# Kernel tuning notes

Hardware: AMD Instinct MI355X
Metric: run time of the kernel (lower is better)

## Reference

```python
import jax, jax.numpy as jnp
import numpy as np

N_EMBD = 1024
N_HEAD = 16
HEAD_DIM = N_EMBD // N_HEAD

def setup_inputs() -> dict:
    key = jax.random.key(0)
    ks = jax.random.split(key, 9)
    B, T, C = 2, 2048, N_EMBD
    s = 1.0 / np.sqrt(C)
    x = jax.random.normal(ks[0], (B, T, C), dtype=jnp.float32)
    Wk = jax.random.normal(ks[1], (C, C), dtype=jnp.float32) * s
    bk = jnp.zeros((C,), dtype=jnp.float32)
    Wq = jax.random.normal(ks[2], (C, C), dtype=jnp.float32) * s
    bq = jnp.zeros((C,), dtype=jnp.float32)
    Wv = jax.random.normal(ks[3], (C, C), dtype=jnp.float32) * s
    bv = jnp.zeros((C,), dtype=jnp.float32)
    Wp = jax.random.normal(ks[4], (C, C), dtype=jnp.float32) * s
    bp = jnp.zeros((C,), dtype=jnp.float32)
    return {"x": x, "Wq": Wq, "bq": bq, "Wk": Wk, "bk": bk, "Wv": Wv, "bv": bv, "Wp": Wp, "bp": bp}

def reference(x, Wq, bq, Wk, bk, Wv, bv, Wp, bp):
    B, T, C = x.shape
    H, D = N_HEAD, HEAD_DIM
    # QKV projections (torch Linear: x @ W.T + b; here W is stored as (in,out))
    q = (x @ Wq + bq).reshape(B, T, H, D).transpose(0, 2, 1, 3)  # [B,H,T,D]
    k = (x @ Wk + bk).reshape(B, T, H, D).transpose(0, 2, 1, 3)
    v = (x @ Wv + bv).reshape(B, T, H, D).transpose(0, 2, 1, 3)
    att = jnp.einsum('bhtd,bhsd->bhts', q, k) / jnp.sqrt(jnp.float32(D))
    causal = jnp.tril(jnp.ones((T, T), dtype=bool))
    att = jnp.where(causal, att, jnp.float32(-jnp.inf))
    att = jax.nn.softmax(att, axis=-1)
    y = jnp.einsum('bhts,bhsd->bhtd', att, v)  # [B,H,T,D]
    y = y.transpose(0, 2, 1, 3).reshape(B, T, C)
    return y @ Wp + bp
```

## Files before the change

### kernel.cpp

```cpp
#include <hip/hip_runtime.h>
#include <cstdint>

typedef __attribute__((ext_vector_type(4))) short s16x4;
typedef __attribute__((ext_vector_type(8))) short s16x8;
typedef __attribute__((ext_vector_type(4))) float f32x4;
typedef __attribute__((ext_vector_type(16))) float f32x16;

#define L2E 1.44269504088896340736f

__device__ __forceinline__ short f2bf(float f) {
  union { float f; unsigned u; } v; v.f = f;
  unsigned r = (v.u + 0x7fffu + ((v.u >> 16) & 1u)) >> 16;
  return (short)r;
}

__device__ __forceinline__ float xhalf_f(float x) {
  union { float f; unsigned u; } a; a.f = x;
  auto r = __builtin_amdgcn_permlane32_swap(a.u, a.u, false, false);
  union { unsigned u; float f; } b;
  b.u = (threadIdx.x & 32) ? r[0] : r[1];
  return b.f;
}

typedef const __attribute__((address_space(1))) unsigned int* gas_p;
typedef __attribute__((address_space(3))) unsigned int* las_p;
__device__ __forceinline__ void stage16(const void* g, void* l) {
  __builtin_amdgcn_global_load_lds((gas_p)(uintptr_t)g,
                                   (las_p)(unsigned int)(uintptr_t)l, 16, 0, 0);
}

__global__ __launch_bounds__(256) void prepass(const float* __restrict__ W0,
                                               const float* __restrict__ W1,
                                               const float* __restrict__ W2,
                                               const float* __restrict__ W3,
                                               short* __restrict__ wdst,
                                               const float* __restrict__ x,
                                               short* __restrict__ xb) {
  const int z = blockIdx.z;
  const int t = threadIdx.x;
  if (z >= 4) {
    int i = ((z - 4) * 256 + blockIdx.y * 16 + blockIdx.x) * 256 + t;
    const f32x4* p = (const f32x4*)x + (size_t)i * 2;
    f32x4 a = p[0], b = p[1];
    s16x8 o;
    o[0] = f2bf(a[0]); o[1] = f2bf(a[1]); o[2] = f2bf(a[2]); o[3] = f2bf(a[3]);
    o[4] = f2bf(b[0]); o[5] = f2bf(b[1]); o[6] = f2bf(b[2]); o[7] = f2bf(b[3]);
    *((s16x8*)xb + i) = o;
    return;
  }
  __shared__ float tile[64][65];
  const float* in = (z == 0) ? W0 : (z == 1) ? W1 : (z == 2) ? W2 : W3;
  short* out = wdst + (size_t)z * 1048576;
  const int bi = blockIdx.y, bj = blockIdx.x;
  const int c = t & 63, r0 = t >> 6;
#pragma unroll
  for (int i = 0; i < 16; i++) {
    int r = r0 + i * 4;
    tile[r][c] = in[(size_t)(bi * 64 + r) * 1024 + bj * 64 + c];
  }
  __syncthreads();
#pragma unroll
  for (int i = 0; i < 16; i++) {
    int r = r0 + i * 4;
    out[(size_t)(bj * 64 + r) * 1024 + bi * 64 + c] = f2bf(tile[c][r]);
  }
}

__global__ __launch_bounds__(512) void gemm_qkv8(
    const short* __restrict__ A, const short* __restrict__ B,
    const float* __restrict__ b0, const float* __restrict__ b1,
    const float* __restrict__ b2, short* __restrict__ o0,
    short* __restrict__ o1, short* __restrict__ o2) {
  constexpr int K = 1024, NKT = 16;
  constexpr int BUFS = 28672;
  __shared__ short L[2 * BUFS];
  const int tid = threadIdx.x;
  const int lane = tid & 63, wave = tid >> 6;
  const int wr = wave >> 2, wc = wave & 3;
  const int l15 = lane & 15, l4 = lane >> 4;
  const int id = blockIdx.x;
  const int wgid = (id & 7) * 32 + (id >> 3);
  const int m0 = (wgid & 15) * 256;
  const int n0 = (wgid >> 4) * 192;
  const short* Asrc = A + (size_t)m0 * K;
  const short* Bsrc = B + (size_t)n0 * K;

  f32x4 acc[8][3];
#pragma unroll
  for (int i = 0; i < 8; i++)
#pragma unroll
    for (int j = 0; j < 3; j++) acc[i][j] = (f32x4){0.f, 0.f, 0.f, 0.f};

  int sALo[2], gALo[2], sBLo[2], gBLo[2];
#pragma unroll
  for (int j = 0; j < 2; j++) {
    const int flat = j * 512 + tid;
    const int r = flat >> 3, ch = flat & 7;
    const int sw8 = ((ch ^ (r & 7)) << 3);
    sALo[j] = (r >> 6) * 8192 + (r & 63) * 64 + (ch << 3);
    gALo[j] = ((r >> 6) * 128 + (r & 63)) * K + sw8;
    sBLo[j] = 16384 + (flat << 3);
    gBLo[j] = r * K + sw8;
  }
  const int rBH = 128 + (tid >> 3), chBH = tid & 7;
  const int sBHi = 16384 + rBH * 64 + (chBH << 3);
  const int gBHi = rBH * K + ((chBH ^ (rBH & 7)) << 3);

  int aoff[2], boff[2];
#pragma unroll
  for (int kf = 0; kf < 2; kf++) {
    const int x = (((kf << 2) + l4) ^ (l15 & 7)) << 3;
    aoff[kf] = wr * 8192 + l15 * 64 + x;
    boff[kf] = 16384 + (wc * 48 + l15) * 64 + x;
  }

#define ST_ALO(BB, T)                                                          \
  { _Pragma("unroll") for (int j_ = 0; j_ < 2; j_++)                           \
        stage16(Asrc + gALo[j_] + (T)*64, L + (BB) + sALo[j_]); }
#define ST_AHI(BB, T)                                                          \
  { _Pragma("unroll") for (int j_ = 0; j_ < 2; j_++)                           \
        stage16(Asrc + gALo[j_] + 64 * K + (T)*64, L + (BB) + sALo[j_] + 4096); }
#define ST_BLO(BB, T)                                                          \
  { _Pragma("unroll") for (int j_ = 0; j_ < 2; j_++)                           \
        stage16(Bsrc + gBLo[j_] + (T)*64, L + (BB) + sBLo[j_]); }
#define ST_BHI(BB, T)                                                          \
  stage16(Bsrc + gBHi + (T)*64, L + (BB) + sBHi);

#define RD_A(MI0)                                                              \
  { _Pragma("unroll") for (int q_ = 0; q_ < 2; q_++)                           \
        _Pragma("unroll") for (int kf_ = 0; kf_ < 2; kf_++)                    \
            af[q_][kf_] = *(const s16x8*)(bc + aoff[kf_] + ((MI0) + q_) * 1024); }

#define BAR_MFMA(MI0)                                                          \
  __builtin_amdgcn_s_barrier();                                                \
  asm volatile("s_waitcnt lgkmcnt(0)" ::: "memory");                           \
  __builtin_amdgcn_sched_barrier(0);                                           \
  __builtin_amdgcn_s_setprio(1);                                               \
  _Pragma("unroll") for (int q_ = 0; q_ < 2; q_++)                             \
      _Pragma("unroll") for (int ni_ = 0; ni_ < 3; ni_++)                      \
          _Pragma("unroll") for (int kf_ = 0; kf_ < 2; kf_++)                  \
              acc[(MI0) + q_][ni_] = __builtin_amdgcn_mfma_f32_16x16x32_bf16(  \
                  af[q_][kf_], bf[ni_][kf_], acc[(MI0) + q_][ni_], 0, 0, 0);   \
  __builtin_amdgcn_s_setprio(0);                                               \
  __builtin_amdgcn_s_barrier();

  ST_ALO(0, 0) ST_AHI(0, 0) ST_BLO(0, 0) ST_BHI(0, 0)
  ST_BLO(BUFS, 1) ST_BHI(BUFS, 1) ST_ALO(BUFS, 1)
  asm volatile("s_waitcnt vmcnt(5)" ::: "memory");
  __builtin_amdgcn_s_barrier();

  int bufc = 0;
  for (int t = 0; t < NKT; ++t) {
    const int bufn = bufc ^ BUFS;
    const short* bc = L + bufc;
    s16x8 bf[3][2], af[2][2];
#pragma unroll
    for (int ni_ = 0; ni_ < 3; ni_++)
#pragma unroll
      for (int kf_ = 0; kf_ < 2; kf_++)
        bf[ni_][kf_] = *(const s16x8*)(bc + boff[kf_] + ni_ * 1024);
    RD_A(0)
    if (t + 1 < NKT) ST_AHI(bufn, t + 1)
    BAR_MFMA(0)
    RD_A(2)
    if (t + 2 < NKT) ST_BLO(bufc, t + 2)
    BAR_MFMA(2)
    RD_A(4)
    if (t + 2 < NKT) ST_BHI(bufc, t + 2)
    BAR_MFMA(4)
    RD_A(6)
    if (t + 2 < NKT) {
      ST_ALO(bufc, t + 2)
      asm volatile("s_waitcnt vmcnt(5)" ::: "memory");
    } else {
      asm volatile("s_waitcnt vmcnt(0)" ::: "memory");
    }
    BAR_MFMA(6)
    bufc = bufn;
  }
#undef ST_ALO
#undef ST_AHI
#undef ST_BLO
#undef ST_BHI
#undef RD_A
#undef BAR_MFMA

#pragma unroll
  for (int ni = 0; ni < 3; ni++) {
    const int col = n0 + wc * 48 + ni * 16 + l15;
    const float* bp; short* dst; int c1; int isV = 0; float scl = 1.0f;
    if (col < 1024) { bp = b0; dst = o0; c1 = col; scl = 0.125f * L2E; }
    else if (col < 2048) { bp = b1; dst = o1; c1 = col - 1024; }
    else { bp = b2; dst = o2; c1 = col - 2048; isV = 1; }
    const float bias = bp[c1];
    const int h = c1 >> 6, d = c1 & 63;
    if (isV) {
#pragma unroll
      for (int mi = 0; mi < 8; mi++) {
        int t0 = m0 + wr * 128 + mi * 16 + l4 * 4;
        int bb = t0 >> 11, tt = t0 & 2047;
        s16x4 ov;
#pragma unroll
        for (int rr = 0; rr < 4; rr++) ov[rr] = f2bf(acc[mi][ni][rr] + bias);
        *(s16x4*)(dst + (size_t)((bb * 16 + h) * 64 + d) * 2048 + tt) = ov;
      }
    } else {
#pragma unroll
      for (int mi = 0; mi < 8; mi++)
#pragma unroll
        for (int rr = 0; rr < 4; rr++) {
          int row = m0 + wr * 128 + mi * 16 + l4 * 4 + rr;
          int bb = row >> 11, tt = row & 2047;
          float v = (acc[mi][ni][rr] + bias) * scl;
          dst[(size_t)((bb * 16 + h) * 2048 + tt) * 64 + d] = f2bf(v);
        }
    }
  }
}

template <int EPI, int BM>
__global__ __launch_bounds__(BM * 2) void gemm_bt(
    const short* __restrict__ A, const short* __restrict__ B, int N, int K,
    const float* __restrict__ b0, float* __restrict__ ofp) {
  constexpr int T = BM * 2;
  constexpr int AR = 2;
  constexpr int BR = 512 / T;
  constexpr int BUFB = (BM + 128) * 32;
  __shared__ short L[2 * BUFB];
  const int tid = threadIdx.x;
  const int lane = tid & 63;
  const int wave = tid >> 6;
  const int wr = wave >> 1, wc = wave & 1;
  const int l15 = lane & 15, l4 = lane >> 4;
  const int id = blockIdx.x + gridDim.x * blockIdx.y;
  const int cpx = gridDim.x >> 3;
  const int xcd = id & 7, sub = id >> 3;
  const int m0 = (sub / cpx) * BM;
  const int n0 = (xcd * cpx + sub % cpx) * 128;
  f32x4 acc[4][4];
#pragma unroll
  for (int i = 0; i < 4; i++)
#pragma unroll
    for (int j = 0; j < 4; j++) acc[i][j] = (f32x4){0.f, 0.f, 0.f, 0.f};

  const int lq = tid & 3, lr = tid >> 2;
  int soffA[AR], goffA[AR];
#pragma unroll
  for (int i = 0; i < AR; i++) {
    const int r = i * (T / 4) + lr;
    soffA[i] = r * 32 + lq * 8;
    goffA[i] = r * K + lq * 8;
  }
  int soffB[BR], goffB[BR];
#pragma unroll
  for (int j = 0; j < BR; j++) {
    const int r = j * (T / 4) + lr;
    soffB[j] = BM * 32 + r * 32 + lq * 8;
    goffB[j] = r * K + lq * 8;
  }

  const short* Asrc = A + (size_t)m0 * K;
  const short* Bsrc = B + (size_t)n0 * K;
  short* bufC = L;
  short* bufN = L + BUFB;

#define GSTAGE(BUF)                                                            \
  {                                                                            \
    _Pragma("unroll") for (int i_ = 0; i_ < AR; i_++)                          \
        stage16(Asrc + goffA[i_], (BUF) + soffA[i_]);                          \
    _Pragma("unroll") for (int j_ = 0; j_ < BR; j_++)                          \
        stage16(Bsrc + goffB[j_], (BUF) + soffB[j_]);                          \
    Asrc += 32; Bsrc += 32;                                                    \
  }

  GSTAGE(bufC)
  const int NK = K >> 5;
  for (int kt = 0; kt < NK; kt++) {
    __syncthreads();
    if (kt + 1 < NK) GSTAGE(bufN)
    s16x8 af[4], bfr[4];
#pragma unroll
    for (int i = 0; i < 4; i++) {
      af[i] = *(const s16x8*)(bufC + (wr * 64 + i * 16 + l15) * 32 + l4 * 8);
      bfr[i] = *(const s16x8*)(bufC + BM * 32 + (wc * 64 + i * 16 + l15) * 32 + l4 * 8);
    }
#pragma unroll
    for (int mi = 0; mi < 4; mi++)
#pragma unroll
      for (int ni = 0; ni < 4; ni++)
        acc[mi][ni] = __builtin_amdgcn_mfma_f32_16x16x32_bf16(af[mi], bfr[ni],
                                                              acc[mi][ni], 0, 0, 0);
    short* t_ = bufC; bufC = bufN; bufN = t_;
  }
#undef GSTAGE

#pragma unroll
  for (int ni = 0; ni < 4; ni++) {
    const int col = n0 + wc * 64 + ni * 16 + l15;
    const float bias = b0[col];
#pragma unroll
    for (int mi = 0; mi < 4; mi++)
#pragma unroll
      for (int r = 0; r < 4; r++) {
        int row = m0 + wr * 64 + mi * 16 + l4 * 4 + r;
        ofp[(size_t)row * N + col] = acc[mi][ni][r] + bias;
      }
  }
}

__global__ __launch_bounds__(128) void attn_v8(const short* __restrict__ Q,
                                               const short* __restrict__ K,
                                               const short* __restrict__ Vt,
                                               short* __restrict__ Y) {
  __shared__ short Ks[2][64 * 64];
  __shared__ short Vs[3][64 * 64];
  const int bh = blockIdx.x;
  const int y = blockIdx.y;
  const int g = y >> 3, r_ = y & 7;
  const int qbase = (g << 3) | ((g & 1) ? (7 - r_) : r_);
  const int qt = (qbase + ((bh & 3) << 3)) & 31;
  const int tid = threadIdx.x, lane = tid & 63, wave = tid >> 6;
  const int q31 = lane & 31, hi = lane >> 5;
  const short* Qp = Q + (size_t)bh * 2048 * 64;
  const short* Kp = K + (size_t)bh * 2048 * 64;
  const short* Vp = Vt + (size_t)bh * 64 * 2048;
  const int qrow = qt * 64 + wave * 32 + q31;
  const int nt = qt + 1;
  const int cx = q31 & 7;

  s16x8 qf[4];
#pragma unroll
  for (int s = 0; s < 4; s++)
    qf[s] = *(const s16x8*)(Qp + (size_t)qrow * 64 + s * 16 + hi * 8);

  f32x16 accA, accB, Z;
#pragma unroll
  for (int i = 0; i < 16; i++) { accA[i] = 0.f; accB[i] = 0.f; Z[i] = 0.f; }
  float l = 0.f;

  const int srow = tid >> 3, sch = tid & 7;
  int sdst[4], koff[4], voff[4];
#pragma unroll
  for (int i = 0; i < 4; i++) {
    const int r = srow + i * 16;
    const int sc = sch ^ (r & 7);
    sdst[i] = r * 64 + sch * 8;
    koff[i] = r * 64 + sc * 8;
    voff[i] = r * 2048 + sc * 8;
  }
  const short* kst = Kp;
  const short* vst = Vp;
  int rd0[4];
#pragma unroll
  for (int s = 0; s < 4; s++) rd0[s] = q31 * 64 + (((2 * s + hi) ^ cx) << 3);

  short* kA = &Ks[0][0]; short* kB = &Ks[1][0];
  short* vP = &Vs[2][0]; short* vC = &Vs[0][0]; short* vN = &Vs[1][0];

#pragma unroll
  for (int i = 0; i < 4; i++) {
    stage16(kst + koff[i], kA + sdst[i]);
    stage16(vst + voff[i], vC + sdst[i]);
  }
  kst += 4096; vst += 64;

#define STAGE_NEXT(COND)                                                       \
  if (COND) {                                                                  \
    _Pragma("unroll") for (int i_ = 0; i_ < 4; i_++) {                         \
      stage16(kst + koff[i_], kB + sdst[i_]);                                  \
      stage16(vst + voff[i_], vN + sdst[i_]);                                  \
    }                                                                          \
    kst += 4096; vst += 64;                                                    \
  }

#define QK(S0, S1)                                                             \
  {                                                                            \
    s16x8 kf0_[4], kf1_[4];                                                    \
    _Pragma("unroll") for (int s_ = 0; s_ < 4; s_++) {                         \
      kf0_[s_] = *(const s16x8*)(kA + rd0[s_]);                                \
      kf1_[s_] = *(const s16x8*)(kA + rd0[s_] + 2048);                         \
    }                                                                          \
    __builtin_amdgcn_s_setprio(1);                                             \
    S0 = __builtin_amdgcn_mfma_f32_32x32x16_bf16(kf0_[0], qf[0], Z, 0, 0, 0);  \
    S1 = __builtin_amdgcn_mfma_f32_32x32x16_bf16(kf1_[0], qf[0], Z, 0, 0, 0);  \
    _Pragma("unroll") for (int s_ = 1; s_ < 4; s_++) {                         \
      S0 = __builtin_amdgcn_mfma_f32_32x32x16_bf16(kf0_[s_], qf[s_], S0, 0, 0, 0); \
      S1 = __builtin_amdgcn_mfma_f32_32x32x16_bf16(kf1_[s_], qf[s_], S1, 0, 0, 0); \
    }                                                                          \
    __builtin_amdgcn_s_setprio(0);                                             \
  }

#define SMPV_BODY(S0, S1)                                                      \
  {                                                                            \
    float rsum_ = 0.f;                                                         \
    _Pragma("unroll") for (int r2_ = 0; r2_ < 16; r2_++) {                     \
      float p_ = __builtin_amdgcn_exp2f(S0[r2_]);                              \
      S0[r2_] = p_; rsum_ += p_;                                               \
    }                                                                          \
    _Pragma("unroll") for (int r2_ = 0; r2_ < 16; r2_++) {                     \
      float p_ = __builtin_amdgcn_exp2f(S1[r2_]);                              \
      S1[r2_] = p_; rsum_ += p_;                                               \
    }                                                                          \
    l += rsum_;                                                                \
    unsigned pk0_[8], pk1_[8];                                                 \
    _Pragma("unroll") for (int j_ = 0; j_ < 8; j_++) {                         \
      unsigned u_;                                                             \
      float a0_ = S0[2 * j_], a1_ = S0[2 * j_ + 1];                            \
      asm("v_cvt_pk_bf16_f32 %0, %1, %2" : "=v"(u_) : "v"(a0_), "v"(a1_));     \
      pk0_[j_] = u_;                                                           \
      float b0_ = S1[2 * j_], b1_ = S1[2 * j_ + 1];                            \
      asm("v_cvt_pk_bf16_f32 %0, %1, %2" : "=v"(u_) : "v"(b0_), "v"(b1_));     \
      pk1_[j_] = u_;                                                           \
    }                                                                          \
    _Pragma("unroll") for (int s_ = 0; s_ < 4; s_++) {                         \
      const unsigned* pk_ = (s_ < 2) ? pk0_ : pk1_;                            \
      const int b_ = 4 * (s_ & 1);                                             \
      auto rA_ = __builtin_amdgcn_permlane32_swap(pk_[b_ + 0], pk_[b_ + 2], false, false); \
      auto rB_ = __builtin_amdgcn_permlane32_swap(pk_[b_ + 1], pk_[b_ + 3], false, false); \
      union { unsigned u[4]; s16x8 v; } fr_;                                   \
      fr_.u[0] = rA_[0]; fr_.u[1] = rB_[0]; fr_.u[2] = rA_[1]; fr_.u[3] = rB_[1]; \
      s16x8 vf0_ = *(const s16x8*)(vP + rd0[s_]);                              \
      s16x8 vf1_ = *(const s16x8*)(vP + rd0[s_] + 2048);                       \
      __builtin_amdgcn_s_setprio(1);                                           \
      accA = __builtin_amdgcn_mfma_f32_32x32x16_bf16(vf0_, fr_.v, accA, 0, 0, 0); \
      accB = __builtin_amdgcn_mfma_f32_32x32x16_bf16(vf1_, fr_.v, accB, 0, 0, 0); \
      __builtin_amdgcn_s_setprio(0);                                           \
    }                                                                          \
  }

#define SMPV_MASK(S0, S1)                                                      \
  {                                                                            \
    const int k0_ = (nt - 1) * 64;                                             \
    _Pragma("unroll") for (int r2_ = 0; r2_ < 16; r2_++) {                     \
      int kvr_ = k0_ + (r2_ & 3) + 8 * (r2_ >> 2) + 4 * hi;                    \
      if (kvr_ > qrow) S0[r2_] = -__builtin_inff();                            \
      if (kvr_ + 32 > qrow) S1[r2_] = -__builtin_inff();                       \
    }                                                                          \
    SMPV_BODY(S0, S1)                                                          \
  }

#define ROT()                                                                  \
  {                                                                            \
    short* t_ = kA; kA = kB; kB = t_;                                          \
    t_ = vP; vP = vC; vC = vN; vN = t_;                                        \
  }

  f32x16 sA0, sA1, sB0, sB1;
  __syncthreads();
  STAGE_NEXT(nt > 1)
  QK(sA0, sA1)
  ROT()
  int t = 1;
  for (; t + 1 < nt; t += 2) {
    __syncthreads();
    STAGE_NEXT(t + 1 < nt)
    QK(sB0, sB1)
    SMPV_BODY(sA0, sA1)
    ROT()
    __syncthreads();
    STAGE_NEXT(t + 2 < nt)
    QK(sA0, sA1)
    SMPV_BODY(sB0, sB1)
    ROT()
  }
  if (t < nt) {
    __syncthreads();
    QK(sB0, sB1)
    SMPV_BODY(sA0, sA1)
    ROT()
    SMPV_MASK(sB0, sB1)
  } else {
    SMPV_MASK(sA0, sA1)
  }
#undef STAGE_NEXT
#undef QK
#undef SMPV_BODY
#undef SMPV_MASK
#undef ROT

  const int b_ = bh >> 4, h_ = bh & 15;
  const float lt = l + xhalf_f(l);
  const float invl = 1.f / lt;
  const size_t base = ((size_t)b_ * 2048 + qrow) * 1024 + h_ * 64;
#pragma unroll
  for (int gg = 0; gg < 4; gg++) {
    s16x4 o0, o1;
#pragma unroll
    for (int e = 0; e < 4; e++) {
      o0[e] = f2bf(accA[4 * gg + e] * invl);
      o1[e] = f2bf(accB[4 * gg + e] * invl);
    }
    *(s16x4*)(Y + base + 8 * gg + 4 * hi) = o0;
    *(s16x4*)(Y + base + 32 + 8 * gg + 4 * hi) = o1;
  }
}

extern "C" void kernel_launch(void* const* d_in, const int* in_sizes, int n_in,
                              void* d_out, int out_size, void* d_ws, size_t ws_size,
                              hipStream_t stream) {
  const float* x = (const float*)d_in[0];
  const float* Wq = (const float*)d_in[1];
  const float* bq = (const float*)d_in[2];
  const float* Wk = (const float*)d_in[3];
  const float* bk = (const float*)d_in[4];
  const float* Wv = (const float*)d_in[5];
  const float* bv = (const float*)d_in[6];
  const float* Wp = (const float*)d_in[7];
  const float* bp = (const float*)d_in[8];
  float* out = (float*)d_out;
  char* ws = (char*)d_ws;

  short* xb    = (short*)(ws + 0);
  short* WqkvT = (short*)(ws + 8388608);
  short* WpT   = (short*)(ws + 14680064);
  short* Qb    = (short*)(ws + 16777216);
  short* Kb    = (short*)(ws + 25165824);
  short* Vtb   = (short*)(ws + 33554432);
  short* Yb    = xb;

  prepass<<<dim3(16, 16, 12), 256, 0, stream>>>(Wq, Wk, Wv, Wp, WqkvT, x, xb);
  gemm_qkv8<<<256, 512, 0, stream>>>(xb, WqkvT, bq, bk, bv, Qb, Kb, Vtb);
  attn_v8<<<dim3(32, 32), 128, 0, stream>>>(Qb, Kb, Vtb, Yb);
  gemm_bt<1, 64><<<dim3(8, 64), 128, 0, stream>>>(Yb, WpT, 1024, 1024, bp, out);
}
```

Measured before the change: 101.1 us.

## Give each wave private K/V LDS buffers and replace block barriers with vmcnt waits

The attention kernel now lets each of the two waves stage its own full copy of every K and V tile into a private LDS region. Block-wide __syncthreads are replaced by per-wave s_waitcnt vmcnt(0), so the waves no longer wait on each other. This removes inter-wave barrier stalls but doubles K/V global load traffic and LDS use per block, which may lower occupancy.

```diff
diff --git a/kernel.cpp b/kernel.cpp
--- a/kernel.cpp
+++ b/kernel.cpp
@@ -308,12 +308,11 @@
   }
 }
 
-__global__ __launch_bounds__(128) void attn_v8(const short* __restrict__ Q,
-                                               const short* __restrict__ K,
-                                               const short* __restrict__ Vt,
-                                               short* __restrict__ Y) {
-  __shared__ short Ks[2][64 * 64];
-  __shared__ short Vs[3][64 * 64];
+__global__ __launch_bounds__(128) void attn_v11(const short* __restrict__ Q,
+                                                const short* __restrict__ K,
+                                                const short* __restrict__ Vt,
+                                                short* __restrict__ Y) {
+  __shared__ short LW[2][20480];
   const int bh = blockIdx.x;
   const int y = blockIdx.y;
   const int g = y >> 3, r_ = y & 7;
@@ -338,15 +337,15 @@
   for (int i = 0; i < 16; i++) { accA[i] = 0.f; accB[i] = 0.f; Z[i] = 0.f; }
   float l = 0.f;
 
-  const int srow = tid >> 3, sch = tid & 7;
-  int sdst[4], koff[4], voff[4];
-#pragma unroll
-  for (int i = 0; i < 4; i++) {
-    const int r = srow + i * 16;
+  const int srow = lane >> 3, sch = lane & 7;
+  int sdst[8], koff[8], voff[8];
+#pragma unroll
+  for (int j = 0; j < 8; j++) {
+    const int r = j * 8 + srow;
     const int sc = sch ^ (r & 7);
-    sdst[i] = r * 64 + sch * 8;
-    koff[i] = r * 64 + sc * 8;
-    voff[i] = r * 2048 + sc * 8;
+    sdst[j] = r * 64 + sch * 8;
+    koff[j] = r * 64 + sc * 8;
+    voff[j] = r * 2048 + sc * 8;
   }
   const short* kst = Kp;
   const short* vst = Vp;
@@ -354,21 +353,25 @@
 #pragma unroll
   for (int s = 0; s < 4; s++) rd0[s] = q31 * 64 + (((2 * s + hi) ^ cx) << 3);
 
-  short* kA = &Ks[0][0]; short* kB = &Ks[1][0];
-  short* vP = &Vs[2][0]; short* vC = &Vs[0][0]; short* vN = &Vs[1][0];
-
-#pragma unroll
-  for (int i = 0; i < 4; i++) {
-    stage16(kst + koff[i], kA + sdst[i]);
-    stage16(vst + voff[i], vC + sdst[i]);
+  short* base = &LW[wave][0];
+  short* kA = base;          short* kB = base + 4096;
+  short* vC = base + 8192;   short* vN = base + 12288;  short* vP = base + 16384;
+
+#pragma unroll
+  for (int j = 0; j < 8; j++) {
+    stage16(kst + koff[j], kA + sdst[j]);
+    stage16(vst + voff[j], vC + sdst[j]);
   }
   kst += 4096; vst += 64;
+
+#define SYNC                                                                   \
+  asm volatile("s_waitcnt vmcnt(0)" ::: "memory");
 
 #define STAGE_NEXT(COND)                                                       \
   if (COND) {                                                                  \
-    _Pragma("unroll") for (int i_ = 0; i_ < 4; i_++) {                         \
-      stage16(kst + koff[i_], kB + sdst[i_]);                                  \
-      stage16(vst + voff[i_], vN + sdst[i_]);                                  \
+    _Pragma("unroll") for (int j_ = 0; j_ < 8; j_++) {                         \
+      stage16(kst + koff[j_], kB + sdst[j_]);                                  \
+      stage16(vst + voff[j_], vN + sdst[j_]);                                  \
     }                                                                          \
     kst += 4096; vst += 64;                                                    \
   }
@@ -446,25 +449,25 @@
   }
 
   f32x16 sA0, sA1, sB0, sB1;
-  __syncthreads();
+  SYNC
   STAGE_NEXT(nt > 1)
   QK(sA0, sA1)
   ROT()
   int t = 1;
   for (; t + 1 < nt; t += 2) {
-    __syncthreads();
+    SYNC
     STAGE_NEXT(t + 1 < nt)
     QK(sB0, sB1)
     SMPV_BODY(sA0, sA1)
     ROT()
-    __syncthreads();
+    SYNC
     STAGE_NEXT(t + 2 < nt)
     QK(sA0, sA1)
     SMPV_BODY(sB0, sB1)
     ROT()
   }
   if (t < nt) {
-    __syncthreads();
+    SYNC
     QK(sB0, sB1)
     SMPV_BODY(sA0, sA1)
     ROT()
@@ -472,6 +475,7 @@
   } else {
     SMPV_MASK(sA0, sA1)
   }
+#undef SYNC
 #undef STAGE_NEXT
 #undef QK
 #undef SMPV_BODY
@@ -481,7 +485,7 @@
   const int b_ = bh >> 4, h_ = bh & 15;
   const float lt = l + xhalf_f(l);
   const float invl = 1.f / lt;
-  const size_t base = ((size_t)b_ * 2048 + qrow) * 1024 + h_ * 64;
+  const size_t base2 = ((size_t)b_ * 2048 + qrow) * 1024 + h_ * 64;
 #pragma unroll
   for (int gg = 0; gg < 4; gg++) {
     s16x4 o0, o1;
@@ -490,8 +494,8 @@
       o0[e] = f2bf(accA[4 * gg + e] * invl);
       o1[e] = f2bf(accB[4 * gg + e] * invl);
     }
-    *(s16x4*)(Y + base + 8 * gg + 4 * hi) = o0;
-    *(s16x4*)(Y + base + 32 + 8 * gg + 4 * hi) = o1;
+    *(s16x4*)(Y + base2 + 8 * gg + 4 * hi) = o0;
+    *(s16x4*)(Y + base2 + 32 + 8 * gg + 4 * hi) = o1;
   }
 }
 
@@ -520,6 +524,6 @@
 
   prepass<<<dim3(16, 16, 12), 256, 0, stream>>>(Wq, Wk, Wv, Wp, WqkvT, x, xb);
   gemm_qkv8<<<256, 512, 0, stream>>>(xb, WqkvT, bq, bk, bv, Qb, Kb, Vtb);
-  attn_v8<<<dim3(32, 32), 128, 0, stream>>>(Qb, Kb, Vtb, Yb);
+  attn_v11<<<dim3(32, 32), 128, 0, stream>>>(Qb, Kb, Vtb, Yb);
   gemm_bt<1, 64><<<dim3(8, 64), 128, 0, stream>>>(Yb, WpT, 1024, 1024, bp, out);
 }
```

Measured after the change: 111.5 us. +10.3%, slower.
